# Optimization experiments

Measured on AMD Instinct MI355X. Metric: run time of the kernel, lower is better.

The kernel has to match this reference:

```python
import jax, jax.numpy as jnp
import numpy as np


def _chord_mask(n):
    # Chord-protocol sparsity: mask[i, i] = 1 and mask[i, (i + 2**j) % n] = 1
    m = np.zeros((n, n), dtype=np.float32)
    idx = np.arange(n)
    m[idx, idx] = 1.0
    for j in range(int(np.log2(n))):
        m[idx, (idx + 2 ** j) % n] = 1.0
    return jnp.asarray(m)


def setup_inputs() -> dict:
    key = jax.random.key(0)
    ks = jax.random.split(key, 8)
    B, n_vec, n_dim = 16, 1024, 64
    n_hidden, n_W, n_class = 32, 10, 10
    data = jax.random.normal(ks[0], (B, n_vec, n_dim), dtype=jnp.float32)
    s1 = 1.0 / np.sqrt(n_dim)
    s2 = 1.0 / np.sqrt(n_hidden)
    s3 = 1.0 / np.sqrt(n_vec * n_dim)
    fW1 = jax.random.uniform(ks[1], (n_W, n_dim, n_hidden), jnp.float32, -s1, s1)
    fb1 = jax.random.uniform(ks[2], (n_W, n_hidden), jnp.float32, -s1, s1)
    fW2 = jax.random.uniform(ks[3], (n_W, n_hidden, n_vec), jnp.float32, -s2, s2)
    fb2 = jax.random.uniform(ks[4], (n_W, n_vec), jnp.float32, -s2, s2)
    final_W = jax.random.uniform(ks[5], (n_vec * n_dim, n_class), jnp.float32, -s3, s3)
    final_b = jax.random.uniform(ks[6], (n_class,), jnp.float32, -s3, s3)
    return {"data": data, "fW1": fW1, "fb1": fb1, "fW2": fW2, "fb2": fb2,
            "final_W": final_W, "final_b": final_b}


def reference(data, fW1, fb1, fW2, fb2, final_W, final_b):
    B, n_vec, n_dim = data.shape
    n_W = fW1.shape[0]
    mask = _chord_mask(n_vec)  # [n_vec, n_vec], static constant
    V = data
    residual = V
    # fs[::-1] -> iterate layers in reverse order
    for i in range(n_W - 1, -1, -1):
        h = jax.nn.gelu(jnp.einsum('bnd,dh->bnh', data, fW1[i]) + fb1[i],
                        approximate=False)
        W = jnp.einsum('bnh,hm->bnm', h, fW2[i]) + fb2[i]  # [B, n_vec, n_vec]
        W = W * mask
        V = jnp.einsum('bnm,bmd->bnd', W, V) + residual
        residual = V  # residual_every=True
    flat = V.reshape(B, n_vec * n_dim)
    return flat @ final_W + final_b
```

## Files before the change

kernel.cpp:

```cpp
#include <hip/hip_runtime.h>

#define BATCH 16
#define NVEC 1024
#define NDIM 64
#define NHID 32
#define NW   10
#define NCLS 10
#define NOFF 11
#define WPAD 12
#define NCHUNK (NDIM / 4)
#define W2PAD 36
#define NROW 16
#define NSLOT 112

__global__ __launch_bounds__(256, 4) void k_weights(
    const float* __restrict__ data,
    const float* __restrict__ fW1,
    const float* __restrict__ fb1,
    const float* __restrict__ fW2,
    const float* __restrict__ fb2,
    float* __restrict__ Wsp)
{
    const int i = blockIdx.y;
    const int nbase = blockIdx.x * NROW;
    const int t = threadIdx.x;
    const int jq = t & 3;
    const int b  = (t >> 2) & 15;
    const int nl = t >> 6;
    const int j0 = jq * 8;

    __shared__ __align__(16) float sW1[NDIM * NHID];
    __shared__ float sb1[NHID];
    __shared__ __align__(16) float sW2r[NSLOT * W2PAD];
    __shared__ float sb2[NSLOT];
    __shared__ __align__(16) float rws[NROW * BATCH * WPAD];

    {
        const float4* w1v = (const float4*)(fW1 + (size_t)i * NDIM * NHID);
        float4* s4 = (float4*)sW1;
        #pragma unroll
        for (int k = t; k < NDIM * NHID / 4; k += 256) s4[k] = w1v[k];
        if (t < NHID) sb1[t] = fb1[i * NHID + t];

        const int j  = t >> 3;
        const int s0 = t & 7;
        const float* w2 = fW2 + ((size_t)i * NHID + j) * NVEC;
        #pragma unroll
        for (int c = 0; c < NSLOT / 8; ++c) {
            int s = s0 + c * 8;
            int k = (s < 32) ? s : ((32 << ((s - 32) >> 4)) + ((s - 32) & 15));
            int m = (nbase + k) & (NVEC - 1);
            sW2r[s * W2PAD + j] = w2[m];
        }
        if (t < NSLOT) {
            int s = t;
            int k = (s < 32) ? s : ((32 << ((s - 32) >> 4)) + ((s - 32) & 15));
            int m = (nbase + k) & (NVEC - 1);
            sb2[s] = fb2[(size_t)i * NVEC + m];
        }
        for (int k = t; k < NROW * BATCH; k += 256) rws[k * WPAD + (WPAD - 1)] = 0.0f;
    }
    __syncthreads();

    float h[4][8];
    #pragma unroll
    for (int r = 0; r < 4; ++r)
        #pragma unroll
        for (int jj = 0; jj < 8; ++jj) h[r][jj] = sb1[j0 + jj];

    const int n0 = nbase + nl * 4;
    const float4* rowp = (const float4*)(data + ((size_t)(b * NVEC) + n0) * NDIM);

    #pragma unroll 2
    for (int g = 0; g < 16; ++g) {
        float4 a0 = rowp[g];
        float4 a1 = rowp[16 + g];
        float4 a2 = rowp[32 + g];
        float4 a3 = rowp[48 + g];
        const float as[4][4] = {{a0.x, a0.y, a0.z, a0.w},
                                {a1.x, a1.y, a1.z, a1.w},
                                {a2.x, a2.y, a2.z, a2.w},
                                {a3.x, a3.y, a3.z, a3.w}};
        #pragma unroll
        for (int dk = 0; dk < 4; ++dk) {
            const float4* wp = (const float4*)(&sW1[(g * 4 + dk) * NHID + j0]);
            float4 w0 = wp[0], w1 = wp[1];
            const float wf[8] = {w0.x, w0.y, w0.z, w0.w, w1.x, w1.y, w1.z, w1.w};
            #pragma unroll
            for (int jj = 0; jj < 8; ++jj) {
                h[0][jj] += as[0][dk] * wf[jj];
                h[1][jj] += as[1][dk] * wf[jj];
                h[2][jj] += as[2][dk] * wf[jj];
                h[3][jj] += as[3][dk] * wf[jj];
            }
        }
    }

    #pragma unroll
    for (int r = 0; r < 4; ++r)
        #pragma unroll
        for (int jj = 0; jj < 8; ++jj) {
            float x = h[r][jj];
            h[r][jj] = 0.5f * x * (1.0f + erff(x * 0.70710678118654752f));
        }

    const int rbase = nl * 4;
    #pragma unroll
    for (int r = 0; r < 4; ++r) {
        #pragma unroll
        for (int o = 0; o < NOFF; ++o) {
            int slot;
            if (o == 0) slot = rbase + r;
            else {
                int off = 1 << (o - 1);
                slot = (off <= 16) ? (rbase + r + off)
                                   : (32 + 16 * (o - 6) + rbase + r);
            }
            const float4* gp = (const float4*)(sW2r + slot * W2PAD + j0);
            float4 g0 = gp[0], g1 = gp[1];
            float w = h[r][0] * g0.x + h[r][1] * g0.y + h[r][2] * g0.z + h[r][3] * g0.w
                    + h[r][4] * g1.x + h[r][5] * g1.y + h[r][6] * g1.z + h[r][7] * g1.w;
            w += __shfl_xor(w, 1, 64);
            w += __shfl_xor(w, 2, 64);
            if (jq == (o & 3))
                rws[(b * NROW + rbase + r) * WPAD + o] = w + sb2[slot];
        }
    }
    __syncthreads();

    {
        const float4* rv = (const float4*)rws;
        #pragma unroll
        for (int k = t; k < NROW * BATCH * 3; k += 256) {
            int row = k / 3, comp = k - row * 3;
            int bb = row >> 4, rr = row & 15;
            float4* dst = (float4*)(Wsp +
                ((size_t)(i * BATCH + bb) * NVEC + nbase + rr) * WPAD + comp * 4);
            *dst = rv[k];
        }
    }
}

__global__ __launch_bounds__(1024) void k_chain(
    const float* __restrict__ data,
    const float* __restrict__ Wsp,
    const float* __restrict__ Wf,
    float* __restrict__ part)
{
    const int lin   = blockIdx.x;
    const int xcd   = lin & 7;
    const int slot  = lin >> 3;
    const int b     = (xcd << 1) | (slot >> 4);
    const int chunk = slot & 15;
    const int d0    = chunk * 4;
    const int n     = threadIdx.x;

    __shared__ float4 bufA[NVEC];
    __shared__ float4 bufB[NVEC];

    float4 vown = *(const float4*)(data + ((size_t)(b * NVEC) + n) * NDIM + d0);
    bufA[n] = vown;

    const float4* wp = (const float4*)(Wsp + ((size_t)((NW - 1) * BATCH + b) * NVEC + n) * WPAD);
    float4 wa = wp[0], wb4 = wp[1], wc = wp[2];
    __syncthreads();

    float4* cur = bufA;
    float4* nxt = bufB;

    for (int l = 0; l < NW; ++l) {
        float4 na, nb, nc;
        if (l < NW - 1) {
            const float4* wpn = (const float4*)(
                Wsp + ((size_t)((NW - 2 - l) * BATCH + b) * NVEC + n) * WPAD);
            na = wpn[0]; nb = wpn[1]; nc = wpn[2];
        }
        const float wgt[12] = {wa.x, wa.y, wa.z, wa.w,
                               wb4.x, wb4.y, wb4.z, wb4.w,
                               wc.x, wc.y, wc.z, wc.w};
        float4 v0 = vown;
        float4 acc;
        acc.x = v0.x + wgt[0] * v0.x;
        acc.y = v0.y + wgt[0] * v0.y;
        acc.z = v0.z + wgt[0] * v0.z;
        acc.w = v0.w + wgt[0] * v0.w;
        #pragma unroll
        for (int o = 1; o < NOFF; ++o) {
            int off = 1 << (o - 1);
            float4 vv = cur[(n + off) & (NVEC - 1)];
            acc.x += wgt[o] * vv.x; acc.y += wgt[o] * vv.y;
            acc.z += wgt[o] * vv.z; acc.w += wgt[o] * vv.w;
        }
        nxt[n] = acc;
        vown = acc;
        __syncthreads();
        float4* tmp = cur; cur = nxt; nxt = tmp;
        if (l < NW - 1) { wa = na; wb4 = nb; wc = nc; }
    }

    float p[NCLS];
    #pragma unroll
    for (int c = 0; c < NCLS; ++c) p[c] = 0.0f;
    {
        float vs[4] = {vown.x, vown.y, vown.z, vown.w};
        const float4* wfv = (const float4*)(Wf + ((size_t)(n * NDIM + d0)) * NCLS);
        float wf[40];
        #pragma unroll
        for (int k = 0; k < 10; ++k) {
            float4 u = wfv[k];
            wf[k * 4 + 0] = u.x; wf[k * 4 + 1] = u.y;
            wf[k * 4 + 2] = u.z; wf[k * 4 + 3] = u.w;
        }
        #pragma unroll
        for (int d = 0; d < 4; ++d)
            #pragma unroll
            for (int cls = 0; cls < NCLS; ++cls)
                p[cls] += vs[d] * wf[d * NCLS + cls];
    }

    const int lane = n & 63, wv = n >> 6;
    float* sred = (float*)nxt;
    #pragma unroll
    for (int cls = 0; cls < NCLS; ++cls) {
        float v = p[cls];
        #pragma unroll
        for (int s = 32; s > 0; s >>= 1) v += __shfl_down(v, s, 64);
        if (lane == 0) sred[wv * NCLS + cls] = v;
    }
    __syncthreads();
    if (n < NCLS) {
        float s = 0.0f;
        #pragma unroll
        for (int w = 0; w < 16; ++w) s += sred[w * NCLS + n];
        part[(size_t)(b * NCHUNK + chunk) * NCLS + n] = s;
    }
}

__global__ __launch_bounds__(256) void k_finish(
    const float* __restrict__ part, const float* __restrict__ bias,
    float* __restrict__ out)
{
    int t = threadIdx.x;
    if (t < BATCH * NCLS) {
        int b = t / NCLS, cls = t % NCLS;
        float s = bias[cls];
        #pragma unroll
        for (int ch = 0; ch < NCHUNK; ++ch)
            s += part[(size_t)(b * NCHUNK + ch) * NCLS + cls];
        out[t] = s;
    }
}

extern "C" void kernel_launch(void* const* d_in, const int* in_sizes, int n_in,
                              void* d_out, int out_size, void* d_ws, size_t ws_size,
                              hipStream_t stream) {
    const float* data = (const float*)d_in[0];
    const float* fW1  = (const float*)d_in[1];
    const float* fb1  = (const float*)d_in[2];
    const float* fW2  = (const float*)d_in[3];
    const float* fb2  = (const float*)d_in[4];
    const float* fWf  = (const float*)d_in[5];
    const float* fbf  = (const float*)d_in[6];
    float* out = (float*)d_out;

    float* ws   = (float*)d_ws;
    float* Wsp  = ws;
    float* part = Wsp + (size_t)NW * BATCH * NVEC * WPAD;

    k_weights<<<dim3(NVEC / NROW, NW), 256, 0, stream>>>(
        data, fW1, fb1, fW2, fb2, Wsp);
    k_chain<<<dim3(NCHUNK * BATCH), 1024, 0, stream>>>(data, Wsp, fWf, part);
    k_finish<<<dim3(1), 256, 0, stream>>>(part, fbf, out);
}
```

Measured before the change: 115.8 us.

## Halve weight-kernel tile and give each chain thread two rows

k_weights now processes 8 rows per block with 128 threads instead of 16 rows with 256 threads. This launches more, smaller blocks, shrinks the shared fW2 slot table, and reorganises the fW2 gather so the loads are coalesced along m. k_chain now uses 512 threads, each handling rows n and n+512. The 512-offset neighbour comes from a register instead of LDS, and there are half as many waves per block to synchronise. The trade-off is more register pressure and less thread-level parallelism per chain block in exchange for fewer LDS reads and cheaper barriers.

```diff
diff --git a/kernel.cpp b/kernel.cpp
--- a/kernel.cpp
+++ b/kernel.cpp
@@ -10,10 +10,10 @@
 #define WPAD 12
 #define NCHUNK (NDIM / 4)
 #define W2PAD 36
-#define NROW 16
-#define NSLOT 112
-
-__global__ __launch_bounds__(256, 4) void k_weights(
+#define NROW 8
+#define NSLOT 64
+
+__global__ __launch_bounds__(128, 2) void k_weights(
     const float* __restrict__ data,
     const float* __restrict__ fW1,
     const float* __restrict__ fb1,
@@ -39,26 +39,20 @@
         const float4* w1v = (const float4*)(fW1 + (size_t)i * NDIM * NHID);
         float4* s4 = (float4*)sW1;
         #pragma unroll
-        for (int k = t; k < NDIM * NHID / 4; k += 256) s4[k] = w1v[k];
+        for (int k = t; k < NDIM * NHID / 4; k += 128) s4[k] = w1v[k];
         if (t < NHID) sb1[t] = fb1[i * NHID + t];
 
-        const int j  = t >> 3;
-        const int s0 = t & 7;
-        const float* w2 = fW2 + ((size_t)i * NHID + j) * NVEC;
-        #pragma unroll
-        for (int c = 0; c < NSLOT / 8; ++c) {
-            int s = s0 + c * 8;
-            int k = (s < 32) ? s : ((32 << ((s - 32) >> 4)) + ((s - 32) & 15));
-            int m = (nbase + k) & (NVEC - 1);
-            sW2r[s * W2PAD + j] = w2[m];
-        }
-        if (t < NSLOT) {
-            int s = t;
-            int k = (s < 32) ? s : ((32 << ((s - 32) >> 4)) + ((s - 32) & 15));
-            int m = (nbase + k) & (NVEC - 1);
-            sb2[s] = fb2[(size_t)i * NVEC + m];
-        }
-        for (int k = t; k < NROW * BATCH; k += 256) rws[k * WPAD + (WPAD - 1)] = 0.0f;
+        const int s  = t & 63;
+        const int j2 = t >> 6;
+        int k = (s < 24) ? s : ((32 << ((s - 24) >> 3)) + ((s - 24) & 7));
+        int m = (nbase + k) & (NVEC - 1);
+        const float* w2 = fW2 + (size_t)i * NHID * NVEC + m;
+        #pragma unroll
+        for (int jj = 0; jj < 16; ++jj)
+            sW2r[s * W2PAD + (j2 + jj * 2)] = w2[(size_t)(j2 + jj * 2) * NVEC];
+        if (t < NSLOT) sb2[s] = fb2[(size_t)i * NVEC + m];
+
+        rws[t * WPAD + (WPAD - 1)] = 0.0f;
     }
     __syncthreads();
 
@@ -114,7 +108,7 @@
             else {
                 int off = 1 << (o - 1);
                 slot = (off <= 16) ? (rbase + r + off)
-                                   : (32 + 16 * (o - 6) + rbase + r);
+                                   : (24 + 8 * (o - 6) + rbase + r);
             }
             const float4* gp = (const float4*)(sW2r + slot * W2PAD + j0);
             float4 g0 = gp[0], g1 = gp[1];
@@ -131,9 +125,9 @@
     {
         const float4* rv = (const float4*)rws;
         #pragma unroll
-        for (int k = t; k < NROW * BATCH * 3; k += 256) {
+        for (int k = t; k < NROW * BATCH * 3; k += 128) {
             int row = k / 3, comp = k - row * 3;
-            int bb = row >> 4, rr = row & 15;
+            int bb = row >> 3, rr = row & 7;
             float4* dst = (float4*)(Wsp +
                 ((size_t)(i * BATCH + bb) * NVEC + nbase + rr) * WPAD + comp * 4);
             *dst = rv[k];
@@ -141,7 +135,7 @@
     }
 }
 
-__global__ __launch_bounds__(1024) void k_chain(
+__global__ __launch_bounds__(512) void k_chain(
     const float* __restrict__ data,
     const float* __restrict__ Wsp,
     const float* __restrict__ Wf,
@@ -154,78 +148,118 @@
     const int chunk = slot & 15;
     const int d0    = chunk * 4;
     const int n     = threadIdx.x;
+    const int n2    = n + 512;
 
     __shared__ float4 bufA[NVEC];
     __shared__ float4 bufB[NVEC];
 
-    float4 vown = *(const float4*)(data + ((size_t)(b * NVEC) + n) * NDIM + d0);
-    bufA[n] = vown;
-
-    const float4* wp = (const float4*)(Wsp + ((size_t)((NW - 1) * BATCH + b) * NVEC + n) * WPAD);
-    float4 wa = wp[0], wb4 = wp[1], wc = wp[2];
+    float4 v0own = *(const float4*)(data + ((size_t)(b * NVEC) + n)  * NDIM + d0);
+    float4 v1own = *(const float4*)(data + ((size_t)(b * NVEC) + n2) * NDIM + d0);
+    bufA[n]  = v0own;
+    bufA[n2] = v1own;
+
+    const float* wbase = Wsp + (size_t)((NW - 1) * BATCH + b) * NVEC * WPAD;
+    const float4* wp0 = (const float4*)(wbase + (size_t)n  * WPAD);
+    const float4* wp1 = (const float4*)(wbase + (size_t)n2 * WPAD);
+    float4 wa0 = wp0[0], wb0 = wp0[1], wc0 = wp0[2];
+    float4 wa1 = wp1[0], wb1 = wp1[1], wc1 = wp1[2];
     __syncthreads();
 
     float4* cur = bufA;
     float4* nxt = bufB;
 
     for (int l = 0; l < NW; ++l) {
-        float4 na, nb, nc;
+        float4 na0, nb0, nc0, na1, nb1, nc1;
         if (l < NW - 1) {
-            const float4* wpn = (const float4*)(
-                Wsp + ((size_t)((NW - 2 - l) * BATCH + b) * NVEC + n) * WPAD);
-            na = wpn[0]; nb = wpn[1]; nc = wpn[2];
-        }
-        const float wgt[12] = {wa.x, wa.y, wa.z, wa.w,
-                               wb4.x, wb4.y, wb4.z, wb4.w,
-                               wc.x, wc.y, wc.z, wc.w};
-        float4 v0 = vown;
-        float4 acc;
-        acc.x = v0.x + wgt[0] * v0.x;
-        acc.y = v0.y + wgt[0] * v0.y;
-        acc.z = v0.z + wgt[0] * v0.z;
-        acc.w = v0.w + wgt[0] * v0.w;
+            const float* nbase_p = Wsp + (size_t)((NW - 2 - l) * BATCH + b) * NVEC * WPAD;
+            const float4* q0 = (const float4*)(nbase_p + (size_t)n  * WPAD);
+            const float4* q1 = (const float4*)(nbase_p + (size_t)n2 * WPAD);
+            na0 = q0[0]; nb0 = q0[1]; nc0 = q0[2];
+            na1 = q1[0]; nb1 = q1[1]; nc1 = q1[2];
+        }
+        const float wg0[12] = {wa0.x, wa0.y, wa0.z, wa0.w,
+                               wb0.x, wb0.y, wb0.z, wb0.w,
+                               wc0.x, wc0.y, wc0.z, wc0.w};
+        const float wg1[12] = {wa1.x, wa1.y, wa1.z, wa1.w,
+                               wb1.x, wb1.y, wb1.z, wb1.w,
+                               wc1.x, wc1.y, wc1.z, wc1.w};
+        float4 acc0;
+        acc0.x = v0own.x + wg0[0] * v0own.x;
+        acc0.y = v0own.y + wg0[0] * v0own.y;
+        acc0.z = v0own.z + wg0[0] * v0own.z;
+        acc0.w = v0own.w + wg0[0] * v0own.w;
         #pragma unroll
         for (int o = 1; o < NOFF; ++o) {
             int off = 1 << (o - 1);
-            float4 vv = cur[(n + off) & (NVEC - 1)];
-            acc.x += wgt[o] * vv.x; acc.y += wgt[o] * vv.y;
-            acc.z += wgt[o] * vv.z; acc.w += wgt[o] * vv.w;
-        }
-        nxt[n] = acc;
-        vown = acc;
+            float4 vv = (off == 512) ? v1own : cur[(n + off) & (NVEC - 1)];
+            acc0.x += wg0[o] * vv.x; acc0.y += wg0[o] * vv.y;
+            acc0.z += wg0[o] * vv.z; acc0.w += wg0[o] * vv.w;
+        }
+        float4 acc1;
+        acc1.x = v1own.x + wg1[0] * v1own.x;
+        acc1.y = v1own.y + wg1[0] * v1own.y;
+        acc1.z = v1own.z + wg1[0] * v1own.z;
+        acc1.w = v1own.w + wg1[0] * v1own.w;
+        #pragma unroll
+        for (int o = 1; o < NOFF; ++o) {
+            int off = 1 << (o - 1);
+            float4 vv = (off == 512) ? v0own : cur[(n2 + off) & (NVEC - 1)];
+            acc1.x += wg1[o] * vv.x; acc1.y += wg1[o] * vv.y;
+            acc1.z += wg1[o] * vv.z; acc1.w += wg1[o] * vv.w;
+        }
+        nxt[n]  = acc0;
+        nxt[n2] = acc1;
+        v0own = acc0;
+        v1own = acc1;
         __syncthreads();
         float4* tmp = cur; cur = nxt; nxt = tmp;
-        if (l < NW - 1) { wa = na; wb4 = nb; wc = nc; }
-    }
-
-    float p[NCLS];
-    #pragma unroll
-    for (int c = 0; c < NCLS; ++c) p[c] = 0.0f;
+        if (l < NW - 1) {
+            wa0 = na0; wb0 = nb0; wc0 = nc0;
+            wa1 = na1; wb1 = nb1; wc1 = nc1;
+        }
+    }
+
+    float p0[NCLS], p1[NCLS];
+    #pragma unroll
+    for (int c = 0; c < NCLS; ++c) { p0[c] = 0.0f; p1[c] = 0.0f; }
     {
-        float vs[4] = {vown.x, vown.y, vown.z, vown.w};
-        const float4* wfv = (const float4*)(Wf + ((size_t)(n * NDIM + d0)) * NCLS);
-        float wf[40];
+        float vs0[4] = {v0own.x, v0own.y, v0own.z, v0own.w};
+        float vs1[4] = {v1own.x, v1own.y, v1own.z, v1own.w};
+        const float4* wfv0 = (const float4*)(Wf + ((size_t)(n  * NDIM + d0)) * NCLS);
+        const float4* wfv1 = (const float4*)(Wf + ((size_t)(n2 * NDIM + d0)) * NCLS);
+        float wf0[40], wf1[40];
         #pragma unroll
         for (int k = 0; k < 10; ++k) {
-            float4 u = wfv[k];
-            wf[k * 4 + 0] = u.x; wf[k * 4 + 1] = u.y;
-            wf[k * 4 + 2] = u.z; wf[k * 4 + 3] = u.w;
+            float4 u0 = wfv0[k], u1 = wfv1[k];
+            wf0[k * 4 + 0] = u0.x; wf0[k * 4 + 1] = u0.y;
+            wf0[k * 4 + 2] = u0.z; wf0[k * 4 + 3] = u0.w;
+            wf1[k * 4 + 0] = u1.x; wf1[k * 4 + 1] = u1.y;
+            wf1[k * 4 + 2] = u1.z; wf1[k * 4 + 3] = u1.w;
         }
         #pragma unroll
         for (int d = 0; d < 4; ++d)
             #pragma unroll
-            for (int cls = 0; cls < NCLS; ++cls)
-                p[cls] += vs[d] * wf[d * NCLS + cls];
+            for (int cls = 0; cls < NCLS; ++cls) {
+                p0[cls] += vs0[d] * wf0[d * NCLS + cls];
+                p1[cls] += vs1[d] * wf1[d * NCLS + cls];
+            }
     }
 
     const int lane = n & 63, wv = n >> 6;
     float* sred = (float*)nxt;
     #pragma unroll
     for (int cls = 0; cls < NCLS; ++cls) {
-        float v = p[cls];
-        #pragma unroll
-        for (int s = 32; s > 0; s >>= 1) v += __shfl_down(v, s, 64);
-        if (lane == 0) sred[wv * NCLS + cls] = v;
+        float v0 = p0[cls];
+        float v1 = p1[cls];
+        #pragma unroll
+        for (int s = 32; s > 0; s >>= 1) {
+            v0 += __shfl_down(v0, s, 64);
+            v1 += __shfl_down(v1, s, 64);
+        }
+        if (lane == 0) {
+            sred[wv * NCLS + cls]       = v0;
+            sred[(wv + 8) * NCLS + cls] = v1;
+        }
     }
     __syncthreads();
     if (n < NCLS) {
@@ -267,8 +301,8 @@
     float* Wsp  = ws;
     float* part = Wsp + (size_t)NW * BATCH * NVEC * WPAD;
 
-    k_weights<<<dim3(NVEC / NROW, NW), 256, 0, stream>>>(
+    k_weights<<<dim3(NVEC / NROW, NW), 128, 0, stream>>>(
         data, fW1, fb1, fW2, fb2, Wsp);
-    k_chain<<<dim3(NCHUNK * BATCH), 1024, 0, stream>>>(data, Wsp, fWf, part);
+    k_chain<<<dim3(NCHUNK * BATCH), 512, 0, stream>>>(data, Wsp, fWf, part);
     k_finish<<<dim3(1), 256, 0, stream>>>(part, fbf, out);
 }
```

New measurement: 115.0 us. Within noise of the previous version (-0.7%).
